# Performance work log

Measured on AMD Instinct MI355X. Metric: run time of the kernel, lower is better.

The kernel has to match this reference:

```python
import jax, jax.numpy as jnp
import numpy as np
from jax import lax

DN = ('NCHW', 'OIHW', 'NCHW')
ROUTE_ITERS = 3
CAPS_NUM, OUT_CAPS, OUT_DIM = 8, 10, 16
IN_CAPS_SIZE = 6 * 6 * 32  # 1152


def _squash(u, axis):
    # Faithful to the repo's (buggy but intentional) squash: mod/(1+mod) * (u/mod_sq)
    mod_sq = jnp.sum(u * u, axis=axis, keepdims=True)
    mod = jnp.sqrt(mod_sq)
    return mod / (1.0 + mod) * (u / mod_sq)


def setup_inputs() -> dict:
    key = jax.random.key(0)
    ks = jax.random.split(key, 6)
    return {
        'x': jax.random.normal(ks[0], (180, 1, 28, 28), jnp.float32),
        'conv1_w': jax.random.normal(ks[1], (256, 1, 9, 9), jnp.float32) * 0.05,
        'conv1_b': jax.random.normal(ks[2], (256,), jnp.float32) * 0.05,
        'caps_w': jax.random.normal(ks[3], (8, 32, 256, 9, 9), jnp.float32) * 0.05,
        'caps_b': jax.random.normal(ks[4], (8, 32), jnp.float32) * 0.05,
        'W_route': jax.random.normal(ks[5], (1, 1152, 10, 16, 8), jnp.float32),
    }


def reference(x, conv1_w, conv1_b, caps_w, caps_b, W_route):
    B = x.shape[0]
    # conv1 + relu: [B,1,28,28] -> [B,256,20,20]
    h = lax.conv_general_dilated(x, conv1_w, (1, 1), 'VALID', dimension_numbers=DN)
    h = jax.nn.relu(h + conv1_b[None, :, None, None])
    # 8 capsule convs fused into one grouped-output conv: -> [B, 8*32, 6, 6]
    kw = caps_w.reshape(CAPS_NUM * 32, 256, 9, 9)
    u = lax.conv_general_dilated(h, kw, (2, 2), 'VALID', dimension_numbers=DN)
    u = u + caps_b.reshape(-1)[None, :, None, None]
    u = u.reshape(B, CAPS_NUM, IN_CAPS_SIZE)          # [B,8,1152]
    u = _squash(u, axis=2)
    # Route: u_hat[b,i,o,d] = sum_k W[0,i,o,d,k] * u[b,k,i]
    ut = jnp.swapaxes(u, 1, 2)                         # [B,1152,8]
    u_hat = jnp.einsum('iodk,bik->biod', W_route[0], ut)  # [B,1152,10,16]
    b_ij = jnp.zeros((IN_CAPS_SIZE, OUT_CAPS), u_hat.dtype)
    v = None
    for _ in range(ROUTE_ITERS):
        c_ij = jax.nn.softmax(b_ij, axis=1)            # softmax over out caps
        s = jnp.einsum('io,biod->bod', c_ij, u_hat)    # [B,10,16]
        # Faithful: original squashes s_j over dim=2 == the out-caps axis (10)
        v = _squash(s, axis=1)                         # [B,10,16]
        uv = jnp.einsum('biod,bod->io', u_hat, v) / B  # mean over batch
        b_ij = b_ij + uv
    return v[..., None]                                # [B,10,16,1]
```

## Files before the change

### kernel.cpp

```cpp
#include <hip/hip_runtime.h>
#include <hip/hip_bf16.h>

#define NB 180
typedef __attribute__((ext_vector_type(8))) short short8;
typedef __attribute__((ext_vector_type(4))) float f32x4;
typedef unsigned short ushort_t;

__device__ __forceinline__ void gload16(const void* src, void* lds_base){
    __builtin_amdgcn_global_load_lds(
        (const __attribute__((address_space(1))) unsigned int*)src,
        (__attribute__((address_space(3))) unsigned int*)lds_base, 16, 0, 0);
}

__device__ __forceinline__ ushort_t f2bu(float v){
    __hip_bfloat16 h = __float2bfloat16(v);
    return *(ushort_t*)&h;
}

__global__ __launch_bounds__(256) void build_bpack_t(const float* __restrict__ w,
                                                     __hip_bfloat16* __restrict__ bpack){
    __shared__ float ls[10368];
    int oc = blockIdx.x, ich = blockIdx.y, t = threadIdx.x;
    const float4* src = (const float4*)(w + (size_t)oc * 20736 + ich * 10368);
    for (int i = t; i < 2592; i += 256) ((float4*)ls)[i] = src[i];
    __syncthreads();
    for (int idx = t; idx < 10368; idx += 256){
        int j = idx & 7, icg = (idx >> 3) & 15, kk = idx >> 7;
        bpack[(size_t)(kk * 32 + ich * 16 + icg) * 2048 + oc * 8 + j] =
            __float2bfloat16(ls[(icg * 8 + j) * 81 + kk]);
    }
}

__global__ __launch_bounds__(256) void build_wpack1(const float* __restrict__ w,
                                                    __hip_bfloat16* __restrict__ wpack1){
    int t = blockIdx.x * 256 + threadIdx.x;
    int j = t & 7, oc = (t >> 3) & 255, gg = t >> 11;
    int k = (gg >> 2) * 32 + (gg & 3) * 8 + j;
    float v = (k < 81) ? w[oc * 81 + k] : 0.f;
    wpack1[t] = __float2bfloat16(v);
}

__global__ __launch_bounds__(256) void build_w2(const float* __restrict__ Wr, float* __restrict__ W2){
    __shared__ float ls[15360];
    int i0 = blockIdx.x * 12, t = threadIdx.x;
    const float4* src = (const float4*)(Wr + (size_t)i0 * 1280);
    for (int w = t; w < 3840; w += 256) ((float4*)ls)[w] = src[w];
    __syncthreads();
    for (int idx = t; idx < 15360; idx += 256){
        int d = idx & 15, r = idx >> 4;
        int il = r % 12, ok = r / 12;
        int k = ok & 7, o = ok >> 3;
        W2[(size_t)o * 147456 + (size_t)(k * 1152 + i0 + il) * 16 + d] =
            ls[il * 1280 + o * 128 + d * 8 + k];
    }
}

__global__ __launch_bounds__(256) void conv1_mfma(const float* __restrict__ x,
                                                  const __hip_bfloat16* __restrict__ wpack1,
                                                  const float* __restrict__ bias,
                                                  __hip_bfloat16* __restrict__ hT){
    __shared__ ushort_t xs[784];
    __shared__ ushort_t ktab[96];
    int bid = blockIdx.x;
    int b = bid >> 2, mc = bid & 3;
    int t = threadIdx.x, lane = t & 63, wn = t >> 6;
    int g = lane >> 4, lr = lane & 15;

    for (int i = t; i < 784; i += 256) xs[i] = f2bu(x[b * 784 + i]);
    if (t < 96) ktab[t] = (t < 81) ? (ushort_t)((t / 9) * 28 + (t % 9)) : (ushort_t)0;
    __syncthreads();

    int p0 = mc * 112;
    int pbm[7];
#pragma unroll
    for (int m = 0; m < 7; m++){
        int p = p0 + m * 16 + lr;
        p = p < 400 ? p : 399;
        pbm[m] = (p / 20) * 28 + (p % 20);
    }

    f32x4 acc[7][4];
#pragma unroll
    for (int m = 0; m < 7; m++)
#pragma unroll
        for (int n = 0; n < 4; n++) acc[m][n] = (f32x4){0.f, 0.f, 0.f, 0.f};

#pragma unroll
    for (int ks = 0; ks < 3; ks++){
        short8 ko = *(const short8*)&ktab[ks * 32 + g * 8];
        short8 bf[4];
#pragma unroll
        for (int n = 0; n < 4; n++)
            bf[n] = *(const short8*)(wpack1 + (size_t)(((ks * 4 + g) * 256) + wn * 64 + n * 16 + lr) * 8);
#pragma unroll
        for (int m = 0; m < 7; m++){
            short8 af;
#pragma unroll
            for (int e = 0; e < 8; e++)
                af[e] = (short)xs[pbm[m] + (int)(ushort_t)ko[e]];
#pragma unroll
            for (int n = 0; n < 4; n++)
                acc[m][n] = __builtin_amdgcn_mfma_f32_16x16x32_bf16(af, bf[n], acc[m][n], 0, 0, 0);
        }
    }

    float bv[4];
#pragma unroll
    for (int n = 0; n < 4; n++) bv[n] = bias[wn * 64 + n * 16 + lr];
#pragma unroll
    for (int m = 0; m < 7; m++){
#pragma unroll
        for (int rg = 0; rg < 4; rg++){
            int p = p0 + m * 16 + g * 4 + rg;
            if (p < 400){
#pragma unroll
                for (int n = 0; n < 4; n++){
                    float v = acc[m][n][rg] + bv[n];
                    v = v > 0.f ? v : 0.f;
                    hT[((size_t)b * 400 + p) * 256 + wn * 64 + n * 16 + lr] = __float2bfloat16(v);
                }
            }
        }
    }
}

__global__ __launch_bounds__(256, 2) void capsconv_mfma(const __hip_bfloat16* __restrict__ hT,
                                                        const __hip_bfloat16* __restrict__ bpack,
                                                        float* __restrict__ part){
    extern __shared__ char smem[];
    ushort_t* hsA = (ushort_t*)smem;

    int mt = blockIdx.x, ky = blockIdx.y, b0 = mt * 4;
    int t = threadIdx.x, lane = t & 63, wn = t >> 6;
    int g = lane >> 4, lr = lane & 15;

    int pfm[9];
#pragma unroll
    for (int m = 0; m < 9; m++){
        int R = m * 16 + lr;
        int lb = R / 36, pos = R - lb * 36;
        int oy = pos / 6, ox = pos - oy * 6;
        int yy = lb * 6 + oy;
        pfm[m] = ((yy * 20 + 2 * ox) << 8) | (ox + 6 * yy);
    }
    int gbase = g * 2048 + wn * 512 + lr * 8;

    auto stageA = [&](int a){
#pragma unroll
        for (int rnd = 0; rnd < 15; rnd++){
            int L = rnd * 256 + t;
            int p = L >> 3, sg = L & 7;
            int yy = p / 20, xx = p - yy * 20;
            int lb = yy / 6;
            int y = ky + 2 * (yy - lb * 6);
            int f = ((xx >> 1) + 6 * yy) & 7;
            const __hip_bfloat16* src = hT + ((size_t)(((b0 + lb) * 20 + y) * 20 + xx) * 256
                                             + a * 64 + 8 * (sg ^ f));
            gload16(src, hsA + (size_t)(rnd * 256 + (t & ~63)) * 8);
        }
    };

    f32x4 acc[9][4];
#pragma unroll
    for (int m = 0; m < 9; m++)
#pragma unroll
        for (int n = 0; n < 4; n++) acc[m][n] = (f32x4){0.f, 0.f, 0.f, 0.f};

    stageA(0);
    __syncthreads();

    for (int a = 0; a < 4; a++){
#pragma unroll 2
        for (int r = 0; r < 18; r++){
            int kx = r >> 1, ics = r & 1;
            int ksg = (ky * 9 + kx) * 8 + 2 * a + ics;
            const __hip_bfloat16* bstep = bpack + (size_t)ksg * 8192 + gbase;
            short8 bf[4];
#pragma unroll
            for (int n = 0; n < 4; n++)
                bf[n] = *(const short8*)(bstep + n * 128);
            int jj = ics * 4 + g;
#pragma unroll
            for (int m = 0; m < 9; m++){
                int pf = pfm[m];
                int p = (pf >> 8) + kx;
                int f = ((pf & 255) + (kx >> 1)) & 7;
                short8 af = *(const short8*)(hsA + (size_t)(p * 8 + (jj ^ f)) * 8);
#pragma unroll
                for (int n = 0; n < 4; n++)
                    acc[m][n] = __builtin_amdgcn_mfma_f32_16x16x32_bf16(af, bf[n], acc[m][n], 0, 0, 0);
            }
        }
        if (a < 3){
            __syncthreads();
            stageA(a + 1);
            __syncthreads();
        }
    }

    float* tl = (float*)smem;
    size_t pbase = ((size_t)ky * 180 + b0) * 9216;
    for (int lb = 0; lb < 4; lb++){
        int rlo = lb * 36;
        __syncthreads();
#pragma unroll
        for (int m = 0; m < 9; m++){
#pragma unroll
            for (int n = 0; n < 4; n++){
                int oc = wn * 64 + n * 16 + lr;
#pragma unroll
                for (int rg = 0; rg < 4; rg++){
                    int row = m * 16 + g * 4 + rg;
                    if (row >= rlo && row < rlo + 36)
                        tl[(row - rlo) * 260 + oc] = acc[m][n][rg];
                }
            }
        }
        __syncthreads();
#pragma unroll
        for (int j = 0; j < 9; j++){
            int pos = j * 4;
            float4 vv;
            vv.x = tl[(pos    ) * 260 + t];
            vv.y = tl[(pos + 1) * 260 + t];
            vv.z = tl[(pos + 2) * 260 + t];
            vv.w = tl[(pos + 3) * 260 + t];
            *(float4*)&part[pbase + (size_t)lb * 9216 + t * 36 + pos] = vv;
        }
    }
}

__global__ __launch_bounds__(192) void reduce_squash_t(const float* __restrict__ part,
                                                       const float* __restrict__ caps_b,
                                                       float* __restrict__ uT){
    __shared__ float red[3];
    int bk = blockIdx.x;
    int b = bk >> 3, k = bk & 7;
    int t = threadIdx.x;
    size_t base = (size_t)k * 1152;
    float vals[6];
    float ssq = 0.f;
#pragma unroll
    for (int j = 0; j < 6; j++){
        int i = t + j * 192;
        int oc = k * 32 + i / 36;
        float v = caps_b[oc];
#pragma unroll
        for (int kyi = 0; kyi < 9; kyi++)
            v += part[(size_t)(kyi * 180 + b) * 9216 + base + i];
        vals[j] = v; ssq += v * v;
    }
#pragma unroll
    for (int off = 32; off; off >>= 1) ssq += __shfl_down(ssq, off, 64);
    if ((t & 63) == 0) red[t >> 6] = ssq;
    __syncthreads();
    float tot = red[0] + red[1] + red[2];
    float scale = 1.f / (sqrtf(tot) + tot);
#pragma unroll
    for (int j = 0; j < 6; j++)
        uT[(base + t + j * 192) * NB + b] = vals[j] * scale;
}

__global__ __launch_bounds__(192) void s_partial2(const float* __restrict__ W2, const float* __restrict__ uT,
                                                  const float* __restrict__ bij, float* __restrict__ part72,
                                                  int first){
    __shared__ float ws2[2048];
    __shared__ float cs[128];
    int o = blockIdx.x, kc = blockIdx.y, t = threadIdx.x;
    const float4* src = (const float4*)(W2 + (size_t)o * 147456 + (size_t)kc * 2048);
    for (int w = t; w < 512; w += 192) ((float4*)ws2)[w] = src[w];
    if (t < 128){
        if (first){
            cs[t] = 0.1f;
        } else {
            int ki = kc * 128 + t;
            int i = ki - (ki / 1152) * 1152;
            const float* bp = bij + (size_t)i * 10;
            float v[10]; float mx = -1e30f;
#pragma unroll
            for (int q = 0; q < 10; q++){ v[q] = bp[q]; mx = fmaxf(mx, v[q]); }
            float sum = 0.f;
#pragma unroll
            for (int q = 0; q < 10; q++){ v[q] = __expf(v[q] - mx); sum += v[q]; }
            cs[t] = v[o] / sum;
        }
    }
    __syncthreads();
    if (t < NB){
        f32x4 a0 = {0,0,0,0}, a1 = {0,0,0,0}, a2 = {0,0,0,0}, a3 = {0,0,0,0};
        const float* up = uT + (size_t)kc * 128 * NB + t;
#pragma unroll 4
        for (int j = 0; j < 128; j++){
            float tmp = up[j * NB] * cs[j];
            const f32x4* wp = (const f32x4*)(ws2 + j * 16);
            a0 += tmp * wp[0]; a1 += tmp * wp[1]; a2 += tmp * wp[2]; a3 += tmp * wp[3];
        }
        f32x4* pp = (f32x4*)(part72 + ((size_t)kc * NB + t) * 160 + o * 16);
        pp[0] = a0; pp[1] = a1; pp[2] = a2; pp[3] = a3;
    }
}

__global__ __launch_bounds__(192) void sred_vsq(const float* __restrict__ part72, float* __restrict__ v){
    __shared__ float sv[160];
    __shared__ float sc[16];
    int b = blockIdx.x, t = threadIdx.x;
    float s = 0.f;
    if (t < 160){
        const float* pp = part72 + (size_t)b * 160 + t;
        for (int kc = 0; kc < 72; kc++)
            s += pp[(size_t)kc * NB * 160];
        sv[t] = s;
    }
    __syncthreads();
    if (t < 16){
        float m = 0.f;
#pragma unroll
        for (int o = 0; o < 10; o++){ float x = sv[o * 16 + t]; m += x * x; }
        sc[t] = 1.f / (sqrtf(m) + m);
    }
    __syncthreads();
    if (t < 160) v[b * 160 + t] = s * sc[t & 15];
}

__global__ __launch_bounds__(320) void p_gemm(const float* __restrict__ uT, const float* __restrict__ v,
                                              float* __restrict__ P){
    __shared__ float vs[60 * 160];
    int t = threadIdx.x;
    int o = t % 10, kil = t / 10;
    int ki = blockIdx.x * 32 + kil;
    float acc[16];
#pragma unroll
    for (int d = 0; d < 16; d++) acc[d] = 0.f;
    const float* up = uT + (size_t)ki * NB;
    for (int b0 = 0; b0 < NB; b0 += 60){
        __syncthreads();
        for (int j = t; j < 9600; j += 320) vs[j] = v[b0 * 160 + j];
        __syncthreads();
        for (int b = 0; b < 60; b++){
            float uv = up[b0 + b];
            const float* vp = &vs[b * 160 + o * 16];
#pragma unroll
            for (int d = 0; d < 16; d++) acc[d] += uv * vp[d];
        }
    }
    float* pp = P + (size_t)ki * 160 + o * 16;
#pragma unroll
    for (int d = 0; d < 16; d++) pp[d] = acc[d];
}

__global__ void uv_contract2(const float* __restrict__ W2, const float* __restrict__ P,
                             float* __restrict__ bij, int first){
    int t = blockIdx.x * 256 + threadIdx.x;
    if (t >= 11520) return;
    int o = t % 10, i = t / 10;
    float acc = 0.f;
    for (int k = 0; k < 8; k++){
        const float4* wp = (const float4*)(W2 + (size_t)o * 147456 + (size_t)(k * 1152 + i) * 16);
        const float4* pp = (const float4*)(P + (size_t)(k * 1152 + i) * 160 + o * 16);
#pragma unroll
        for (int q = 0; q < 4; q++){
            float4 a = wp[q], b = pp[q];
            acc += a.x * b.x + a.y * b.y + a.z * b.z + a.w * b.w;
        }
    }
    float val = acc * (1.0f / 180.0f);
    bij[t] = first ? val : bij[t] + val;
}

extern "C" void kernel_launch(void* const* d_in, const int* in_sizes, int n_in,
                              void* d_out, int out_size, void* d_ws, size_t ws_size,
                              hipStream_t stream){
    const float* x       = (const float*)d_in[0];
    const float* conv1_w = (const float*)d_in[1];
    const float* conv1_b = (const float*)d_in[2];
    const float* caps_w  = (const float*)d_in[3];
    const float* caps_b  = (const float*)d_in[4];
    const float* Wr      = (const float*)d_in[5];
    float* out = (float*)d_out;

    char* wsb = (char*)d_ws;
    __hip_bfloat16* hTb   = (__hip_bfloat16*)wsb;
    __hip_bfloat16* bpack = (__hip_bfloat16*)(wsb + 36864000);
    float* part = (float*)(wsb + 36864000 + 10616832);
    float* uT   = part + 14929920;
    __hip_bfloat16* wpack1 = (__hip_bfloat16*)(wsb + 113836032);

    float* W2     = part;
    float* part72 = W2 + 1474560;
    float* P      = part72 + 2073600;
    float* bij    = P + 1474560;

    hipFuncSetAttribute((const void*)capsconv_mfma,
                        hipFuncAttributeMaxDynamicSharedMemorySize, 65536);

    build_bpack_t<<<dim3(256, 2), 256, 0, stream>>>(caps_w, bpack);
    build_wpack1<<<96, 256, 0, stream>>>(conv1_w, wpack1);
    conv1_mfma<<<720, 256, 0, stream>>>(x, wpack1, conv1_b, hTb);
    capsconv_mfma<<<dim3(45, 9), 256, 61440, stream>>>(hTb, bpack, part);
    reduce_squash_t<<<1440, 192, 0, stream>>>(part, caps_b, uT);
    build_w2<<<96, 256, 0, stream>>>(Wr, W2);

    for (int it = 0; it < 3; ++it){
        s_partial2<<<dim3(10, 72), 192, 0, stream>>>(W2, uT, bij, part72, it == 0 ? 1 : 0);
        sred_vsq<<<180, 192, 0, stream>>>(part72, out);
        if (it < 2){
            p_gemm<<<288, 320, 0, stream>>>(uT, out, P);
            uv_contract2<<<45, 256, 0, stream>>>(W2, P, bij, it == 0 ? 1 : 0);
        }
    }
}
```

Before: 316.0 us.

## Remap capsconv blocks across XCDs and split squash output transpose into tiled kernel

The capsule conv grid becomes a 1D launch of 408 blocks whose IDs are remapped so that consecutive (mt, ky) tiles land on the same XCD (bid&7 selects a chunk of 51), with three padding blocks exiting early. The point is better L2 locality for shared hT and bpack data. The reduce-squash kernel now writes u in batch-major order with coalesced stores, and a new 32x32 LDS-tiled transpose kernel produces uT. This replaces the strided scatter writes, at the cost of an extra launch and an extra round trip through memory.

```diff
diff --git a/kernel.cpp b/kernel.cpp
--- a/kernel.cpp
+++ b/kernel.cpp
@@ -130,7 +130,11 @@
     extern __shared__ char smem[];
     ushort_t* hsA = (ushort_t*)smem;
 
-    int mt = blockIdx.x, ky = blockIdx.y, b0 = mt * 4;
+    int bid = blockIdx.x;
+    int idx = (bid & 7) * 51 + (bid >> 3);
+    if (idx >= 405) return;
+    int mt = idx / 9, ky = idx - mt * 9;
+    int b0 = mt * 4;
     int t = threadIdx.x, lane = t & 63, wn = t >> 6;
     int g = lane >> 4, lr = lane & 15;
 
@@ -230,9 +234,9 @@
     }
 }
 
-__global__ __launch_bounds__(192) void reduce_squash_t(const float* __restrict__ part,
-                                                       const float* __restrict__ caps_b,
-                                                       float* __restrict__ uT){
+__global__ __launch_bounds__(192) void reduce_squash(const float* __restrict__ part,
+                                                     const float* __restrict__ caps_b,
+                                                     float* __restrict__ u){
     __shared__ float red[3];
     int bk = blockIdx.x;
     int b = bk >> 3, k = bk & 7;
@@ -258,7 +262,18 @@
     float scale = 1.f / (sqrtf(tot) + tot);
 #pragma unroll
     for (int j = 0; j < 6; j++)
-        uT[(base + t + j * 192) * NB + b] = vals[j] * scale;
+        u[(size_t)b * 9216 + base + t + j * 192] = vals[j] * scale;
+}
+
+__global__ __launch_bounds__(1024) void transpose_u(const float* __restrict__ u, float* __restrict__ uT){
+    __shared__ float tile[32][33];
+    int ki0 = blockIdx.x * 32, b0 = blockIdx.y * 32;
+    int tx = threadIdx.x, ty = threadIdx.y;
+    int b = b0 + ty;
+    if (b < NB) tile[ty][tx] = u[(size_t)b * 9216 + ki0 + tx];
+    __syncthreads();
+    int bw = b0 + tx;
+    if (bw < NB) uT[(size_t)(ki0 + ty) * NB + bw] = tile[tx][ty];
 }
 
 __global__ __launch_bounds__(192) void s_partial2(const float* __restrict__ W2, const float* __restrict__ uT,
@@ -382,8 +397,9 @@
     __hip_bfloat16* hTb   = (__hip_bfloat16*)wsb;
     __hip_bfloat16* bpack = (__hip_bfloat16*)(wsb + 36864000);
     float* part = (float*)(wsb + 36864000 + 10616832);
-    float* uT   = part + 14929920;
-    __hip_bfloat16* wpack1 = (__hip_bfloat16*)(wsb + 113836032);
+    float* u    = part + 14929920;
+    float* uT   = u + 1658880;
+    __hip_bfloat16* wpack1 = (__hip_bfloat16*)((char*)(uT + 1658880));
 
     float* W2     = part;
     float* part72 = W2 + 1474560;
@@ -396,8 +412,9 @@
     build_bpack_t<<<dim3(256, 2), 256, 0, stream>>>(caps_w, bpack);
     build_wpack1<<<96, 256, 0, stream>>>(conv1_w, wpack1);
     conv1_mfma<<<720, 256, 0, stream>>>(x, wpack1, conv1_b, hTb);
-    capsconv_mfma<<<dim3(45, 9), 256, 61440, stream>>>(hTb, bpack, part);
-    reduce_squash_t<<<1440, 192, 0, stream>>>(part, caps_b, uT);
+    capsconv_mfma<<<408, 256, 61440, stream>>>(hTb, bpack, part);
+    reduce_squash<<<1440, 192, 0, stream>>>(part, caps_b, u);
+    transpose_u<<<dim3(288, 6), dim3(32, 32), 0, stream>>>(u, uT);
     build_w2<<<96, 256, 0, stream>>>(Wr, W2);
 
     for (int it = 0; it < 3; ++it){
```

Measured after the change: 307.8 us. 1.03x faster.
